# Kernel optimization log

Hardware: AMD Instinct MI355X
Metric: run time of the kernel (lower is better)

## Reference

```python
import jax, jax.numpy as jnp
import numpy as np

EMBED = 1024
N_HEAD = 16
HEAD_DIM = EMBED // N_HEAD


def setup_inputs() -> dict:
    key = jax.random.key(0)
    ks = jax.random.split(key, 9)
    def xavier(k, shape, fan_in, fan_out):
        bound = float(np.sqrt(6.0 / (fan_in + fan_out)))
        return jax.random.uniform(k, shape, jnp.float32, -bound, bound)
    x = jax.random.normal(ks[0], (4, 2048, EMBED), jnp.float32)
    wq = xavier(ks[1], (N_HEAD, EMBED, HEAD_DIM), EMBED, HEAD_DIM)
    wk = xavier(ks[2], (N_HEAD, EMBED, HEAD_DIM), EMBED, HEAD_DIM)
    wv = xavier(ks[3], (N_HEAD, EMBED, HEAD_DIM), EMBED, HEAD_DIM)
    bq = jnp.zeros((N_HEAD, 1, HEAD_DIM), jnp.float32)
    bk = jnp.zeros((N_HEAD, 1, HEAD_DIM), jnp.float32)
    bv = jnp.zeros((N_HEAD, 1, HEAD_DIM), jnp.float32)
    # nn.Linear default init: uniform(-1/sqrt(in), 1/sqrt(in)), weight [out, in]
    bnd = 1.0 / float(np.sqrt(EMBED))
    wo = jax.random.uniform(ks[4], (EMBED, EMBED), jnp.float32, -bnd, bnd)
    bo = jax.random.uniform(ks[5], (EMBED,), jnp.float32, -bnd, bnd)
    return {"x": x, "wq": wq, "bq": bq, "wk": wk, "bk": bk,
            "wv": wv, "bv": bv, "wo": wo, "bo": bo}


def reference(x, wq, bq, wk, bk, wv, bv, wo, bo):
    # per-head projections: [b,s,d] x [h,d,e] -> [b,h,s,e]
    q = jnp.einsum('bsd,hde->bhse', x, wq) + bq
    k = jnp.einsum('bsd,hde->bhse', x, wk) + bk
    v = jnp.einsum('bsd,hde->bhse', x, wv) + bv
    scale = 1.0 / jnp.sqrt(jnp.asarray(q.shape[-1], q.dtype))
    scores = jax.nn.softmax(jnp.einsum('bhse,bhte->bhst', q, k) * scale, axis=-1)
    att = jnp.einsum('bhst,bhte->bhse', scores, v)  # [b,h,s,e]
    b, h, s, e = att.shape
    att = att.transpose(0, 2, 1, 3).reshape(b, s, h * e)
    return att @ wo.T + bo
```

## Files before the change

kernel.cpp:

```cpp
#include <hip/hip_runtime.h>
#include <hip/hip_bf16.h>
#include <stdint.h>

typedef __attribute__((ext_vector_type(8))) short short8;
typedef __attribute__((ext_vector_type(4))) short short4v;
typedef __attribute__((ext_vector_type(4))) float f32x4;
typedef __attribute__((ext_vector_type(4))) float float4v;

#define LOG2E_OVER8 0.18033688011112042f

__device__ __forceinline__ short bf16r(float f) {
  union { float f; uint32_t u; } v; v.f = f;
  uint32_t r = (v.u + 0x7FFFu + ((v.u >> 16) & 1u)) >> 16;
  return (short)r;
}

__device__ __forceinline__ void gload16(const void* g, void* l) {
  __builtin_amdgcn_global_load_lds((const __attribute__((address_space(1))) void*)g,
                                   (__attribute__((address_space(3))) void*)l, 16, 0, 0);
}

__global__ void k_prep(const float* __restrict__ x, const float* __restrict__ wo,
                       const float* __restrict__ wq, const float* __restrict__ wk,
                       const float* __restrict__ wv,
                       short* __restrict__ xb, short* __restrict__ wob,
                       short* __restrict__ wt) {
  __shared__ short tile[64][65];
  int bid = blockIdx.x;
  int tid = threadIdx.x;
  if (bid < 8192) {
    int i = bid * 256 + tid;
    float4v v = *(const float4v*)(x + (size_t)i * 4);
    short4v o = { bf16r(v[0]), bf16r(v[1]), bf16r(v[2]), bf16r(v[3]) };
    *(short4v*)(xb + (size_t)i * 4) = o;
  } else if (bid < 9216) {
    int i = (bid - 8192) * 256 + tid;
    float4v v = *(const float4v*)(wo + (size_t)i * 4);
    short4v o = { bf16r(v[0]), bf16r(v[1]), bf16r(v[2]), bf16r(v[3]) };
    *(short4v*)(wob + (size_t)i * 4) = o;
  } else {
    int b2 = bid - 9216;
    int kt = b2 & 15, h = (b2 >> 4) & 15, wsel = b2 >> 8;
    const float* src = wsel == 0 ? wq : (wsel == 1 ? wk : wv);
    {
      int e = tid & 63, r4 = tid >> 6;
#pragma unroll
      for (int p = 0; p < 16; ++p) {
        int kk = p * 4 + r4;
        tile[kk][e] = bf16r(src[h * 65536 + (kt * 64 + kk) * 64 + e]);
      }
    }
    __syncthreads();
    {
      int kk = tid & 63, r4 = tid >> 6;
#pragma unroll
      for (int p = 0; p < 16; ++p) {
        int e = p * 4 + r4;
        wt[(size_t)(wsel * 1024 + h * 64 + e) * 1024 + kt * 64 + kk] = tile[kk][e];
      }
    }
  }
}

template<int EPI>
__global__ __launch_bounds__(256, 2) void k_gemm(
    const short* __restrict__ A, const short* __restrict__ Bt,
    const float* __restrict__ b0, const float* __restrict__ b1, const float* __restrict__ b2,
    short* __restrict__ qb, short* __restrict__ kb, short* __restrict__ vtb,
    float* __restrict__ outp) {
  __shared__ short smem[16384];
  short* Asb = smem;
  short* Bsb = smem + 8192;
  int tid = threadIdx.x;
  int l = tid & 63, w = tid >> 6;
  int g = l >> 4, c = l & 15;
  int wm = w >> 1, wn = w & 1;
  const int NBX = (EPI == 0) ? 24 : 8;
  const int nwg = NBX * 64;
  int orig = blockIdx.x + blockIdx.y * NBX;
  int swz = (orig & 7) * (nwg >> 3) + (orig >> 3);
  int m0 = (swz / NBX) * 128, n0 = (swz % NBX) * 128;

  f32x4 acc[4][4];
#pragma unroll
  for (int i = 0; i < 4; ++i)
#pragma unroll
    for (int j = 0; j < 4; ++j) acc[i][j] = (f32x4){0.f, 0.f, 0.f, 0.f};

  auto stage = [&](int buf, int kt) {
#pragma unroll
    for (int i = 0; i < 2; ++i) {
      int ch = w * 128 + i * 64 + l;
      int row = ch >> 2, cbs = ch & 3;
      int sb = cbs ^ ((row >> 1) & 3);
      gload16(A + (size_t)(m0 + row) * 1024 + kt * 32 + sb * 8,
              &Asb[buf * 4096 + (w * 128 + i * 64) * 8]);
      gload16(Bt + (size_t)(n0 + row) * 1024 + kt * 32 + sb * 8,
              &Bsb[buf * 4096 + (w * 128 + i * 64) * 8]);
    }
  };

  stage(0, 0);
  __syncthreads();
  for (int kt = 0; kt < 32; ++kt) {
    int buf = kt & 1;
    if (kt + 1 < 32) stage(buf ^ 1, kt + 1);
    short8 af[4], bfr[4];
#pragma unroll
    for (int mi = 0; mi < 4; ++mi) {
      int row = wm * 64 + mi * 16 + c;
      int blk = g ^ ((row >> 1) & 3);
      af[mi] = *(const short8*)&Asb[buf * 4096 + row * 32 + blk * 8];
    }
#pragma unroll
    for (int ni = 0; ni < 4; ++ni) {
      int row = wn * 64 + ni * 16 + c;
      int blk = g ^ ((row >> 1) & 3);
      bfr[ni] = *(const short8*)&Bsb[buf * 4096 + row * 32 + blk * 8];
    }
#pragma unroll
    for (int mi = 0; mi < 4; ++mi)
#pragma unroll
      for (int ni = 0; ni < 4; ++ni)
        acc[mi][ni] = __builtin_amdgcn_mfma_f32_16x16x32_bf16(af[mi], bfr[ni], acc[mi][ni], 0, 0, 0);
    __syncthreads();
  }

  if (EPI == 0 && n0 >= 2048) {
#pragma unroll
    for (int mi = 0; mi < 4; ++mi)
#pragma unroll
      for (int ni = 0; ni < 4; ++ni) {
        int ln = wn * 64 + ni * 16 + c;
        float bias = b2[(n0 - 2048) + ln];
        int ls0 = wm * 64 + mi * 16 + g * 4;
        int blk = ls0 >> 3;
        int sblk = blk ^ (ln & 15);
        short4v o;
#pragma unroll
        for (int r = 0; r < 4; ++r) o[r] = bf16r(acc[mi][ni][r] + bias);
        *(short4v*)&smem[ln * 128 + sblk * 8 + (ls0 & 7)] = o;
      }
    __syncthreads();
    int b = m0 >> 11, s0g = m0 & 2047;
    int h0 = (n0 - 2048) >> 6;
    int vrow0 = (b * 16 + h0) * 64;
#pragma unroll
    for (int p = 0; p < 8; ++p) {
      int ln = p * 16 + (tid >> 4);
      int L = tid & 15;
      int tp = L >> 3, B = L & 7;
      int sa0 = tp * 64 + (B >> 2) * 32 + (B & 3) * 4;
      int sb0 = sa0 + 16;
      int blka = ((sa0 >> 3) ^ (ln & 15)) * 8 + (sa0 & 7);
      int blkb = ((sb0 >> 3) ^ (ln & 15)) * 8 + (sb0 & 7);
      short4v va = *(const short4v*)&smem[ln * 128 + blka];
      short4v vb = *(const short4v*)&smem[ln * 128 + blkb];
      short8 v = {va[0], va[1], va[2], va[3], vb[0], vb[1], vb[2], vb[3]};
      *(short8*)&vtb[(size_t)(vrow0 + ln) * 2048 + s0g + L * 8] = v;
    }
    return;
  }

#pragma unroll
  for (int mi = 0; mi < 4; ++mi)
#pragma unroll
    for (int ni = 0; ni < 4; ++ni) {
      int n = n0 + wn * 64 + ni * 16 + c;
      if (EPI == 0) {
        int sel = n >> 10, nn = n & 1023;
        int h = nn >> 6, e = nn & 63;
        const float* bp = sel == 0 ? b0 : b1;
        short* dst = sel == 0 ? qb : kb;
        float bias = bp[nn];
        float sc = (sel == 0) ? LOG2E_OVER8 : 1.0f;
#pragma unroll
        for (int r = 0; r < 4; ++r) {
          int m = m0 + wm * 64 + mi * 16 + g * 4 + r;
          int b = m >> 11, s = m & 2047;
          float v = (acc[mi][ni][r] + bias) * sc;
          dst[(size_t)((b * 16 + h) * 2048 + s) * 64 + e] = bf16r(v);
        }
      } else {
        float bias = b0[n];
#pragma unroll
        for (int r = 0; r < 4; ++r) {
          int m = m0 + wm * 64 + mi * 16 + g * 4 + r;
          outp[(size_t)m * 1024 + n] = acc[mi][ni][r] + bias;
        }
      }
    }
}

__global__ __launch_bounds__(256, 4) void k_attn(
    const short* __restrict__ Qb, const short* __restrict__ Kb,
    const short* __restrict__ Vt, short* __restrict__ attb) {
  __shared__ short Ks[2][64 * 64];
  __shared__ short Vs[2][64 * 64];
  int tid = threadIdx.x;
  int l = tid & 63, w = tid >> 6;
  int g = l >> 4, c = l & 15;
  int orig = blockIdx.x + blockIdx.y * 16;
  int swz = (orig & 7) * 128 + (orig >> 3);
  int qt = swz & 15, bh = swz >> 4;
  int q0 = qt * 128 + w * 32;

  const short* Qh = Qb + (size_t)bh * 2048 * 64;
  short8 qf[2][2];
#pragma unroll
  for (int qi = 0; qi < 2; ++qi)
#pragma unroll
    for (int es = 0; es < 2; ++es)
      qf[qi][es] = *(const short8*)&Qh[(size_t)(q0 + qi * 16 + c) * 64 + es * 32 + g * 8];

  int koff[4][2];
#pragma unroll
  for (int mi = 0; mi < 4; ++mi) {
    int row = mi * 16 + c;
    koff[mi][0] = row * 64 + ((g ^ (row & 7)) * 8);
    koff[mi][1] = row * 64 + (((4 + g) ^ (row & 7)) * 8);
  }
  int voff[2][4];
#pragma unroll
  for (int ks = 0; ks < 2; ++ks)
#pragma unroll
    for (int ei = 0; ei < 4; ++ei) {
      int row = ei * 16 + c;
      voff[ks][ei] = row * 64 + (((ks * 4 + g) ^ (row & 7)) * 8);
    }

  const short* kptr[2];
  const short* vptr[2];
  int ldst[2];
#pragma unroll
  for (int i = 0; i < 2; ++i) {
    int ch = w * 128 + i * 64 + l;
    int row = ch >> 3, cbs = ch & 7;
    int sb = cbs ^ (row & 7);
    kptr[i] = Kb + (size_t)(bh * 2048 + row) * 64 + sb * 8;
    vptr[i] = Vt + (size_t)(bh * 64 + row) * 2048 + sb * 8;
    ldst[i] = (w * 128 + i * 64) * 8;
  }

  const f32x4 z4 = (f32x4){0.f, 0.f, 0.f, 0.f};
  f32x4 oacc[4][2];
#pragma unroll
  for (int i = 0; i < 4; ++i) { oacc[i][0] = z4; oacc[i][1] = z4; }
  f32x4 lsum[2] = {z4, z4};

  const short one_bf16 = (short)0x3F80;
  const short8 ones = {one_bf16, one_bf16, one_bf16, one_bf16,
                       one_bf16, one_bf16, one_bf16, one_bf16};

  auto stageKV = [&](int buf) {
#pragma unroll
    for (int i = 0; i < 2; ++i) {
      gload16(kptr[i], &Ks[buf][ldst[i]]);
      gload16(vptr[i], &Vs[buf][ldst[i]]);
      kptr[i] += 64 * 64;
      vptr[i] += 64;
    }
  };

  stageKV(0);
  __syncthreads();

  for (int t = 0; t < 32; ++t) {
    int buf = t & 1;
    if (t + 1 < 32) stageKV(buf ^ 1);

    const short* Kbuf = &Ks[buf][0];
    short8 kf0[4], kf1[4];
#pragma unroll
    for (int mi = 0; mi < 4; ++mi) {
      kf0[mi] = *(const short8*)&Kbuf[koff[mi][0]];
      kf1[mi] = *(const short8*)&Kbuf[koff[mi][1]];
    }
    f32x4 sacc[4][2];
    __builtin_amdgcn_s_setprio(1);
#pragma unroll
    for (int mi = 0; mi < 4; ++mi)
#pragma unroll
      for (int qi = 0; qi < 2; ++qi)
        sacc[mi][qi] = __builtin_amdgcn_mfma_f32_16x16x32_bf16(kf0[mi], qf[qi][0], z4, 0, 0, 0);
#pragma unroll
    for (int mi = 0; mi < 4; ++mi)
#pragma unroll
      for (int qi = 0; qi < 2; ++qi)
        sacc[mi][qi] = __builtin_amdgcn_mfma_f32_16x16x32_bf16(kf1[mi], qf[qi][1], sacc[mi][qi], 0, 0, 0);
    __builtin_amdgcn_s_setprio(0);

    short8 pf[2][2];
#pragma unroll
    for (int qi = 0; qi < 2; ++qi) {
      float p[4][4];
#pragma unroll
      for (int mi = 0; mi < 4; ++mi)
#pragma unroll
        for (int r = 0; r < 4; ++r)
          p[mi][r] = __builtin_amdgcn_exp2f(sacc[mi][qi][r]);
#pragma unroll
      for (int ks = 0; ks < 2; ++ks) {
        union { uint32_t w[4]; short8 s; } pu;
        asm("v_cvt_pk_bf16_f32 %0, %1, %2" : "=v"(pu.w[0]) : "v"(p[ks * 2][0]), "v"(p[ks * 2][1]));
        asm("v_cvt_pk_bf16_f32 %0, %1, %2" : "=v"(pu.w[1]) : "v"(p[ks * 2][2]), "v"(p[ks * 2][3]));
        asm("v_cvt_pk_bf16_f32 %0, %1, %2" : "=v"(pu.w[2]) : "v"(p[ks * 2 + 1][0]), "v"(p[ks * 2 + 1][1]));
        asm("v_cvt_pk_bf16_f32 %0, %1, %2" : "=v"(pu.w[3]) : "v"(p[ks * 2 + 1][2]), "v"(p[ks * 2 + 1][3]));
        pf[qi][ks] = pu.s;
      }
    }

    const short* Vbuf = &Vs[buf][0];
    __builtin_amdgcn_s_setprio(1);
#pragma unroll
    for (int qi = 0; qi < 2; ++qi)
#pragma unroll
      for (int ks = 0; ks < 2; ++ks)
        lsum[qi] = __builtin_amdgcn_mfma_f32_16x16x32_bf16(ones, pf[qi][ks], lsum[qi], 0, 0, 0);
#pragma unroll
    for (int ks = 0; ks < 2; ++ks)
#pragma unroll
      for (int ei = 0; ei < 4; ++ei) {
        short8 vf = *(const short8*)&Vbuf[voff[ks][ei]];
#pragma unroll
        for (int qi = 0; qi < 2; ++qi)
          oacc[ei][qi] = __builtin_amdgcn_mfma_f32_16x16x32_bf16(vf, pf[qi][ks], oacc[ei][qi], 0, 0, 0);
      }
    __builtin_amdgcn_s_setprio(0);

    __syncthreads();
  }

  int b = bh >> 4, h = bh & 15;
#pragma unroll
  for (int qi = 0; qi < 2; ++qi) {
    float inv = 1.0f / lsum[qi][0];
    int s = q0 + qi * 16 + c;
#pragma unroll
    for (int ei = 0; ei < 4; ++ei) {
      short4v o;
#pragma unroll
      for (int r = 0; r < 4; ++r) o[r] = bf16r(oacc[ei][qi][r] * inv);
      *(short4v*)&attb[(size_t)(b * 2048 + s) * 1024 + h * 64 + ei * 16 + g * 4] = o;
    }
  }
}

extern "C" void kernel_launch(void* const* d_in, const int* in_sizes, int n_in,
                              void* d_out, int out_size, void* d_ws, size_t ws_size,
                              hipStream_t stream) {
  const float* x  = (const float*)d_in[0];
  const float* wq = (const float*)d_in[1];
  const float* bq = (const float*)d_in[2];
  const float* wk = (const float*)d_in[3];
  const float* bk = (const float*)d_in[4];
  const float* wv = (const float*)d_in[5];
  const float* bv = (const float*)d_in[6];
  const float* wo = (const float*)d_in[7];
  const float* bo = (const float*)d_in[8];
  float* out = (float*)d_out;

  uint8_t* ws = (uint8_t*)d_ws;
  short* xb  = (short*)(ws);
  short* wt  = (short*)(ws + (16u << 20));
  short* wob = (short*)(ws + (22u << 20));
  short* qb  = (short*)(ws + (24u << 20));
  short* kb  = (short*)(ws + (40u << 20));
  short* vtb = (short*)(ws + (56u << 20));
  short* attb = xb;

  k_prep<<<9984, 256, 0, stream>>>(x, wo, wq, wk, wv, xb, wob, wt);
  k_gemm<0><<<dim3(24, 64), 256, 0, stream>>>(xb, wt, bq, bk, bv, qb, kb, vtb, nullptr);
  k_attn<<<dim3(16, 64), 256, 0, stream>>>(qb, kb, vtb, attb);
  k_gemm<1><<<dim3(8, 64), 256, 0, stream>>>(attb, wob, bo, nullptr, nullptr,
                                             nullptr, nullptr, nullptr, out);
}
```

Before: 174.8 us.

## Use 256x128 GEMM tiles with triple-buffered LDS and interleaved prefetch

The GEMM kernel's tile grows from 128x128 to 256x128, so each wave owns an 8x4 grid of MFMA blocks and B-tile reuse per wave doubles. The double-buffered staging with a full __syncthreads per K-step becomes a three-stage LDS ring that prefetches two steps ahead. Global-to-LDS loads are interleaved between the MFMA halves, waits use partial vmcnt counts, and setprio raises wave priority around the MFMA blocks. The trade-off is higher register and LDS use, which lowers occupancy, and half as many workgroups, which may leave some of the GPU's compute units idle.

```diff
diff --git a/kernel.cpp b/kernel.cpp
--- a/kernel.cpp
+++ b/kernel.cpp
@@ -68,105 +68,155 @@
     const float* __restrict__ b0, const float* __restrict__ b1, const float* __restrict__ b2,
     short* __restrict__ qb, short* __restrict__ kb, short* __restrict__ vtb,
     float* __restrict__ outp) {
-  __shared__ short smem[16384];
-  short* Asb = smem;
-  short* Bsb = smem + 8192;
+  __shared__ short smem[36864];
   int tid = threadIdx.x;
   int l = tid & 63, w = tid >> 6;
   int g = l >> 4, c = l & 15;
-  int wm = w >> 1, wn = w & 1;
+  int wr = w >> 1, wc = w & 1;
   const int NBX = (EPI == 0) ? 24 : 8;
-  const int nwg = NBX * 64;
+  const int nwg = NBX * 32;
   int orig = blockIdx.x + blockIdx.y * NBX;
   int swz = (orig & 7) * (nwg >> 3) + (orig >> 3);
-  int m0 = (swz / NBX) * 128, n0 = (swz % NBX) * 128;
-
-  f32x4 acc[4][4];
-#pragma unroll
-  for (int i = 0; i < 4; ++i)
+  int m0 = (swz / NBX) * 256, n0 = (swz % NBX) * 128;
+
+  f32x4 acc[8][4];
+#pragma unroll
+  for (int i = 0; i < 8; ++i)
 #pragma unroll
     for (int j = 0; j < 4; ++j) acc[i][j] = (f32x4){0.f, 0.f, 0.f, 0.f};
 
-  auto stage = [&](int buf, int kt) {
-#pragma unroll
-    for (int i = 0; i < 2; ++i) {
-      int ch = w * 128 + i * 64 + l;
-      int row = ch >> 2, cbs = ch & 3;
-      int sb = cbs ^ ((row >> 1) & 3);
-      gload16(A + (size_t)(m0 + row) * 1024 + kt * 32 + sb * 8,
-              &Asb[buf * 4096 + (w * 128 + i * 64) * 8]);
-      gload16(Bt + (size_t)(n0 + row) * 1024 + kt * 32 + sb * 8,
-              &Bsb[buf * 4096 + (w * 128 + i * 64) * 8]);
-    }
-  };
-
-  stage(0, 0);
-  __syncthreads();
+  int aoff[8], boff[4];
+#pragma unroll
+  for (int mi = 0; mi < 8; ++mi) {
+    int R = wr * 128 + mi * 16 + c;
+    aoff[mi] = R * 32 + ((g ^ ((R >> 1) & 3)) * 8);
+  }
+#pragma unroll
+  for (int ni = 0; ni < 4; ++ni) {
+    int R = wc * 64 + ni * 16 + c;
+    boff[ni] = R * 32 + ((g ^ ((R >> 1) & 3)) * 8);
+  }
+
+  const short* asrc[4]; int adst[4];
+  const short* bsrc[2]; int bdst[2];
+#pragma unroll
+  for (int i = 0; i < 4; ++i) {
+    int ch = i * 256 + tid;
+    int row = ch >> 2, cbs = ch & 3;
+    int sb = cbs ^ ((row >> 1) & 3);
+    asrc[i] = A + (size_t)(m0 + row) * 1024 + sb * 8;
+    adst[i] = ch * 8;
+  }
+#pragma unroll
+  for (int i = 0; i < 2; ++i) {
+    int ch = i * 256 + tid;
+    int row = ch >> 2, cbs = ch & 3;
+    int sb = cbs ^ ((row >> 1) & 3);
+    bsrc[i] = Bt + (size_t)(n0 + row) * 1024 + sb * 8;
+    bdst[i] = ch * 8;
+  }
+
+#pragma unroll
+  for (int i = 0; i < 4; ++i) gload16(asrc[i], &smem[adst[i]]);
+#pragma unroll
+  for (int i = 0; i < 2; ++i) gload16(bsrc[i], &smem[24576 + bdst[i]]);
+#pragma unroll
+  for (int i = 0; i < 4; ++i) gload16(asrc[i] + 32, &smem[8192 + adst[i]]);
+#pragma unroll
+  for (int i = 0; i < 2; ++i) gload16(bsrc[i] + 32, &smem[24576 + 4096 + bdst[i]]);
+  asm volatile("s_waitcnt vmcnt(6)" ::: "memory");
+  __builtin_amdgcn_s_barrier();
+
+  int cur = 0;
   for (int kt = 0; kt < 32; ++kt) {
-    int buf = kt & 1;
-    if (kt + 1 < 32) stage(buf ^ 1, kt + 1);
-    short8 af[4], bfr[4];
-#pragma unroll
-    for (int mi = 0; mi < 4; ++mi) {
-      int row = wm * 64 + mi * 16 + c;
-      int blk = g ^ ((row >> 1) & 3);
-      af[mi] = *(const short8*)&Asb[buf * 4096 + row * 32 + blk * 8];
-    }
-#pragma unroll
-    for (int ni = 0; ni < 4; ++ni) {
-      int row = wn * 64 + ni * 16 + c;
-      int blk = g ^ ((row >> 1) & 3);
-      bfr[ni] = *(const short8*)&Bsb[buf * 4096 + row * 32 + blk * 8];
-    }
+    int stg = cur + 2; if (stg >= 3) stg -= 3;
+    const short* Ab = &smem[cur * 8192];
+    const short* Bb = &smem[24576 + cur * 4096];
+    bool pre = (kt + 2 < 32);
+    int ko = (kt + 2) * 32;
+
+    short8 af0[4], bf[4];
+#pragma unroll
+    for (int mi = 0; mi < 4; ++mi) af0[mi] = *(const short8*)&Ab[aoff[mi]];
+#pragma unroll
+    for (int ni = 0; ni < 4; ++ni) bf[ni] = *(const short8*)&Bb[boff[ni]];
+    if (pre) {
+      gload16(asrc[0] + ko, &smem[stg * 8192 + adst[0]]);
+      gload16(asrc[1] + ko, &smem[stg * 8192 + adst[1]]);
+      gload16(bsrc[0] + ko, &smem[24576 + stg * 4096 + bdst[0]]);
+    }
+    __builtin_amdgcn_s_setprio(1);
 #pragma unroll
     for (int mi = 0; mi < 4; ++mi)
 #pragma unroll
       for (int ni = 0; ni < 4; ++ni)
-        acc[mi][ni] = __builtin_amdgcn_mfma_f32_16x16x32_bf16(af[mi], bfr[ni], acc[mi][ni], 0, 0, 0);
+        acc[mi][ni] = __builtin_amdgcn_mfma_f32_16x16x32_bf16(af0[mi], bf[ni], acc[mi][ni], 0, 0, 0);
+    __builtin_amdgcn_s_setprio(0);
+
+    short8 af1[4];
+#pragma unroll
+    for (int mi = 0; mi < 4; ++mi) af1[mi] = *(const short8*)&Ab[aoff[mi + 4]];
+    if (pre) {
+      gload16(asrc[2] + ko, &smem[stg * 8192 + adst[2]]);
+      gload16(asrc[3] + ko, &smem[stg * 8192 + adst[3]]);
+      gload16(bsrc[1] + ko, &smem[24576 + stg * 4096 + bdst[1]]);
+    }
+    __builtin_amdgcn_s_setprio(1);
+#pragma unroll
+    for (int mi = 0; mi < 4; ++mi)
+#pragma unroll
+      for (int ni = 0; ni < 4; ++ni)
+        acc[mi + 4][ni] = __builtin_amdgcn_mfma_f32_16x16x32_bf16(af1[mi], bf[ni], acc[mi + 4][ni], 0, 0, 0);
+    __builtin_amdgcn_s_setprio(0);
+
+    if (kt < 31) {
+      if (kt < 30) asm volatile("s_waitcnt vmcnt(6)" ::: "memory");
+      else         asm volatile("s_waitcnt vmcnt(0)" ::: "memory");
+      __builtin_amdgcn_s_barrier();
+    }
+    cur = cur + 1; if (cur == 3) cur = 0;
+  }
+
+  if (EPI == 0 && n0 >= 2048) {
     __syncthreads();
-  }
-
-  if (EPI == 0 && n0 >= 2048) {
-#pragma unroll
-    for (int mi = 0; mi < 4; ++mi)
+#pragma unroll
+    for (int mi = 0; mi < 8; ++mi)
 #pragma unroll
       for (int ni = 0; ni < 4; ++ni) {
-        int ln = wn * 64 + ni * 16 + c;
+        int ln = wc * 64 + ni * 16 + c;
         float bias = b2[(n0 - 2048) + ln];
-        int ls0 = wm * 64 + mi * 16 + g * 4;
+        int ls0 = wr * 128 + mi * 16 + g * 4;
         int blk = ls0 >> 3;
-        int sblk = blk ^ (ln & 15);
+        int sblk = blk ^ (ln & 31);
         short4v o;
 #pragma unroll
         for (int r = 0; r < 4; ++r) o[r] = bf16r(acc[mi][ni][r] + bias);
-        *(short4v*)&smem[ln * 128 + sblk * 8 + (ls0 & 7)] = o;
+        *(short4v*)&smem[ln * 256 + sblk * 8 + (ls0 & 7)] = o;
       }
     __syncthreads();
     int b = m0 >> 11, s0g = m0 & 2047;
     int h0 = (n0 - 2048) >> 6;
     int vrow0 = (b * 16 + h0) * 64;
 #pragma unroll
-    for (int p = 0; p < 8; ++p) {
-      int ln = p * 16 + (tid >> 4);
-      int L = tid & 15;
-      int tp = L >> 3, B = L & 7;
-      int sa0 = tp * 64 + (B >> 2) * 32 + (B & 3) * 4;
+    for (int p = 0; p < 16; ++p) {
+      int ln = p * 8 + (tid >> 5);
+      int L2 = tid & 31;
+      int T = L2 >> 3, B = L2 & 7;
+      int sa0 = T * 64 + (B >> 2) * 32 + (B & 3) * 4;
       int sb0 = sa0 + 16;
-      int blka = ((sa0 >> 3) ^ (ln & 15)) * 8 + (sa0 & 7);
-      int blkb = ((sb0 >> 3) ^ (ln & 15)) * 8 + (sb0 & 7);
-      short4v va = *(const short4v*)&smem[ln * 128 + blka];
-      short4v vb = *(const short4v*)&smem[ln * 128 + blkb];
+      short4v va = *(const short4v*)&smem[ln * 256 + ((sa0 >> 3) ^ (ln & 31)) * 8 + (sa0 & 7)];
+      short4v vb = *(const short4v*)&smem[ln * 256 + ((sb0 >> 3) ^ (ln & 31)) * 8 + (sb0 & 7)];
       short8 v = {va[0], va[1], va[2], va[3], vb[0], vb[1], vb[2], vb[3]};
-      *(short8*)&vtb[(size_t)(vrow0 + ln) * 2048 + s0g + L * 8] = v;
+      *(short8*)&vtb[(size_t)(vrow0 + ln) * 2048 + s0g + L2 * 8] = v;
     }
     return;
   }
 
 #pragma unroll
-  for (int mi = 0; mi < 4; ++mi)
+  for (int mi = 0; mi < 8; ++mi)
 #pragma unroll
     for (int ni = 0; ni < 4; ++ni) {
-      int n = n0 + wn * 64 + ni * 16 + c;
+      int n = n0 + wc * 64 + ni * 16 + c;
       if (EPI == 0) {
         int sel = n >> 10, nn = n & 1023;
         int h = nn >> 6, e = nn & 63;
@@ -176,7 +226,7 @@
         float sc = (sel == 0) ? LOG2E_OVER8 : 1.0f;
 #pragma unroll
         for (int r = 0; r < 4; ++r) {
-          int m = m0 + wm * 64 + mi * 16 + g * 4 + r;
+          int m = m0 + wr * 128 + mi * 16 + g * 4 + r;
           int b = m >> 11, s = m & 2047;
           float v = (acc[mi][ni][r] + bias) * sc;
           dst[(size_t)((b * 16 + h) * 2048 + s) * 64 + e] = bf16r(v);
@@ -185,7 +235,7 @@
         float bias = b0[n];
 #pragma unroll
         for (int r = 0; r < 4; ++r) {
-          int m = m0 + wm * 64 + mi * 16 + g * 4 + r;
+          int m = m0 + wr * 128 + mi * 16 + g * 4 + r;
           outp[(size_t)m * 1024 + n] = acc[mi][ni][r] + bias;
         }
       }
@@ -370,8 +420,8 @@
   short* attb = xb;
 
   k_prep<<<9984, 256, 0, stream>>>(x, wo, wq, wk, wv, xb, wob, wt);
-  k_gemm<0><<<dim3(24, 64), 256, 0, stream>>>(xb, wt, bq, bk, bv, qb, kb, vtb, nullptr);
+  k_gemm<0><<<dim3(24, 32), 256, 0, stream>>>(xb, wt, bq, bk, bv, qb, kb, vtb, nullptr);
   k_attn<<<dim3(16, 64), 256, 0, stream>>>(qb, kb, vtb, attb);
-  k_gemm<1><<<dim3(8, 64), 256, 0, stream>>>(attb, wob, bo, nullptr, nullptr,
+  k_gemm<1><<<dim3(8, 32), 256, 0, stream>>>(attb, wob, bo, nullptr, nullptr,
                                              nullptr, nullptr, nullptr, out);
 }
```

Result: faster. 161.8 us (-7.4%).
